# Kernel tuning notes

Hardware: AMD Instinct MI355X
Metric: run time of the kernel (lower is better)

Reference implementation:

```python
import jax, jax.numpy as jnp
import numpy as np

B, T, A, OBS = 4096, 32, 4, 115
H, K, ACT = 64, 8, 19
FEAT = 4 + 3 + 4 * A          # 23 structured features
IN_DIM = FEAT + ACT * A       # 99 with action one-hots


def setup_inputs() -> dict:
    key = jax.random.key(0)
    ks = jax.random.split(key, 16)
    s = lambda *sh: 1.0 / np.sqrt(sh[-1])
    inp = {
        "obs_seq": jax.random.normal(ks[0], (B, T, A, OBS), jnp.float32),
        "action_seq": jax.random.randint(ks[1], (B, T, A), 0, ACT, jnp.int32),
        # feature_proj: Linear(IN_DIM->H) + LayerNorm(H)
        "proj_W": jax.random.normal(ks[2], (H, IN_DIM), jnp.float32) * s(H, IN_DIM),
        "proj_b": jnp.zeros((H,), jnp.float32),
        "ln_g": jnp.ones((H,), jnp.float32),
        "ln_b": jnp.zeros((H,), jnp.float32),
        # 2-layer GRU
        "Wih0": jax.random.normal(ks[3], (3 * H, H), jnp.float32) * s(1, H),
        "Whh0": jax.random.normal(ks[4], (3 * H, H), jnp.float32) * s(1, H),
        "bih0": jnp.zeros((3 * H,), jnp.float32),
        "bhh0": jnp.zeros((3 * H,), jnp.float32),
        "Wih1": jax.random.normal(ks[5], (3 * H, H), jnp.float32) * s(1, H),
        "Whh1": jax.random.normal(ks[6], (3 * H, H), jnp.float32) * s(1, H),
        "bih1": jnp.zeros((3 * H,), jnp.float32),
        "bhh1": jnp.zeros((3 * H,), jnp.float32),
        # classifier MLP
        "cls_W1": jax.random.normal(ks[7], (H, H), jnp.float32) * s(H, H),
        "cls_b1": jnp.zeros((H,), jnp.float32),
        "cls_W2": jax.random.normal(ks[8], (K, H), jnp.float32) * s(K, H),
        "cls_b2": jnp.zeros((K,), jnp.float32),
    }
    return inp


def _extract_features(obs_seq, action_seq):
    b, t, a = obs_seq.shape[:3]
    # ball position from player 0's obs, and its finite-difference velocity
    ball_pos = obs_seq[:, :, 0, 88:90]                       # [B,T,2]
    ball_vel = jnp.concatenate(
        [jnp.zeros_like(ball_pos[:, :1]), ball_pos[:, 1:] - ball_pos[:, :-1]], axis=1)
    pos = obs_seq[..., 0:2]                                   # [B,T,A,2]
    pos_flat = pos.reshape(b, t, a * 2)
    centroid = pos.mean(axis=2)                               # [B,T,2]
    spread = jnp.sqrt(((pos - centroid[:, :, None]) ** 2).sum(-1).mean(2, keepdims=True) + 1e-6)
    # closest-teammate relative position: vectorized argmin over pairwise dists
    diff = pos[:, :, :, None, :] - pos[:, :, None, :, :]      # [B,T,A,A,2]
    d2 = (diff ** 2).sum(-1)                                  # [B,T,A,A]
    d2 = jnp.where(jnp.eye(a, dtype=bool), jnp.inf, d2)       # exclude self
    idx = jnp.argmin(d2, axis=-1)                             # [B,T,A]
    nearest = jnp.take_along_axis(pos, idx[..., None], axis=2)  # [B,T,A,2]
    closest_rel = (nearest - pos).reshape(b, t, a * 2)
    onehot = jax.nn.one_hot(action_seq, ACT, dtype=jnp.float32).reshape(b, t, a * ACT)
    return jnp.concatenate(
        [ball_pos, ball_vel, pos_flat, centroid, spread, closest_rel, onehot], axis=-1)


def _gru_layer(x_tbh, Wih, Whh, bih, bhh):
    h0 = jnp.zeros((x_tbh.shape[1], Whh.shape[1]), x_tbh.dtype)

    def step(h, x):
        gi = x @ Wih.T + bih
        gh = h @ Whh.T + bhh
        ir, iz, inn = jnp.split(gi, 3, axis=-1)
        hr, hz, hn = jnp.split(gh, 3, axis=-1)
        r = jax.nn.sigmoid(ir + hr)
        z = jax.nn.sigmoid(iz + hz)
        n = jnp.tanh(inn + r * hn)
        h_new = (1.0 - z) * n + z * h
        return h_new, h_new

    h_last, ys = jax.lax.scan(step, h0, x_tbh)
    return ys, h_last


def reference(obs_seq, action_seq, proj_W, proj_b, ln_g, ln_b,
              Wih0, Whh0, bih0, bhh0, Wih1, Whh1, bih1, bhh1,
              cls_W1, cls_b1, cls_W2, cls_b2):
    feats = _extract_features(obs_seq, action_seq)            # [B,T,99]
    x = feats @ proj_W.T + proj_b                             # [B,T,H]
    mu = x.mean(-1, keepdims=True)
    var = x.var(-1, keepdims=True)
    x = (x - mu) * jax.lax.rsqrt(var + 1e-5) * ln_g + ln_b
    x = jax.nn.relu(x)
    x = jnp.swapaxes(x, 0, 1)                                 # [T,B,H]
    ys0, _ = _gru_layer(x, Wih0, Whh0, bih0, bhh0)
    _, h_last = _gru_layer(ys0, Wih1, Whh1, bih1, bhh1)       # [B,H]
    hid = jax.nn.relu(h_last @ cls_W1.T + cls_b1)
    logits = hid @ cls_W2.T + cls_b2                          # [B,K]
    return logits
```

## Files before the change

### kernel.cpp

```cpp
#include <hip/hip_runtime.h>

#define B_ 4096
#define T_ 32
#define A_ 4
#define OBS_ 115
#define H_ 64
#define IN_DIM_ 99
#define ACT_ 19
#define NBT (B_*T_)

typedef _Float16 f16;
typedef _Float16 f16x8 __attribute__((ext_vector_type(8)));
typedef float f32x4 __attribute__((ext_vector_type(4)));

static __device__ __forceinline__ float sigmoid_f(float x) {
    return __builtin_amdgcn_rcpf(1.f + __expf(-x));
}
static __device__ __forceinline__ float tanh_f(float x) {
    return 1.f - 2.f * __builtin_amdgcn_rcpf(1.f + __expf(2.f * x));
}
static __device__ __forceinline__ f32x4 mfma16(f16x8 a, f16x8 b, f32x4 c) {
    return __builtin_amdgcn_mfma_f32_16x16x32_f16(a, b, c, 0, 0, 0);
}

__global__ __launch_bounds__(512, 1) void fused_all(
        const float* __restrict__ obs, const int* __restrict__ act,
        const float* __restrict__ projW, const float* __restrict__ pb,
        const float* __restrict__ lng, const float* __restrict__ lnb,
        const float* __restrict__ Wih0, const float* __restrict__ Whh0,
        const float* __restrict__ bih0, const float* __restrict__ bhh0,
        const float* __restrict__ Wih1, const float* __restrict__ Whh1,
        const float* __restrict__ bih1, const float* __restrict__ bhh1,
        const float* __restrict__ W1, const float* __restrict__ b1,
        const float* __restrict__ W2, const float* __restrict__ b2,
        float* __restrict__ out) {
    __shared__ float fl[512 * 25];
    __shared__ float wtl[IN_DIM_ * 64];
    __shared__ int al[512];
    __shared__ __align__(16) f16 xls[32 * 16 * 72];
    __shared__ __align__(16) f16 hbuf[2][2][16 * 72];

    int tid = threadIdx.x;
    int lane = tid & 63;
    int wv = __builtin_amdgcn_readfirstlane(tid >> 6);
    int c = lane & 15, q = lane >> 4;
    int rowbase = blockIdx.x * 16;

    auto ldw = [&](const float* W, int row0, int kcol) -> f16x8 {
        const float* p = W + (size_t)(row0 + c) * 64 + kcol + q * 8;
        f32x4 w0 = *(const f32x4*)p;
        f32x4 w1 = *(const f32x4*)(p + 4);
        f16x8 r;
        r[0] = (f16)w0[0]; r[1] = (f16)w0[1]; r[2] = (f16)w0[2]; r[3] = (f16)w0[3];
        r[4] = (f16)w1[0]; r[5] = (f16)w1[1]; r[6] = (f16)w1[2]; r[7] = (f16)w1[3];
        return r;
    };
    int L = wv >> 2;
    int S = (wv & 3) * 16;
    const float* Wih = L ? Wih1 : Wih0;
    const float* Whh = L ? Whh1 : Whh0;
    const float* bih = L ? bih1 : bih0;
    const float* bhh = L ? bhh1 : bhh0;
    f16x8 wih[3][2], whh[3][2];
#pragma unroll
    for (int g = 0; g < 3; g++)
#pragma unroll
        for (int kf = 0; kf < 2; kf++) {
            wih[g][kf] = ldw(Wih, g * 64 + S, kf * 32);
            whh[g][kf] = ldw(Whh, g * 64 + S, kf * 32);
        }
    float br = bih[S + c] + bhh[S + c];
    float bz = bih[64 + S + c] + bhh[64 + S + c];
    float bi = bih[128 + S + c];
    float bh = bhh[128 + S + c];
    f32x4 vbr = {br, br, br, br}, vbz = {bz, bz, bz, bz};
    f32x4 vbi = {bi, bi, bi, bi}, vbh = {bh, bh, bh, bh};

    {
        int n = blockIdx.x * 512 + tid;
        const float* o = obs + (size_t)n * (A_ * OBS_);
        float px[A_], py[A_];
#pragma unroll
        for (int a = 0; a < A_; a++) {
            float2 p2 = *(const float2*)&o[a * OBS_];
            px[a] = p2.x; py[a] = p2.y;
        }
        float2 bl = *(const float2*)&o[88];
        int t0 = tid & 31;
        float2 pbl = bl;
        if (t0 > 0) pbl = *(const float2*)&o[88 - A_ * OBS_];

        float cx = (px[0] + px[1] + px[2] + px[3]) * 0.25f;
        float cy = (py[0] + py[1] + py[2] + py[3]) * 0.25f;
        float sp = 0.f;
#pragma unroll
        for (int a = 0; a < A_; a++) { float dx = px[a] - cx, dy = py[a] - cy; sp += dx * dx + dy * dy; }
        sp = sqrtf(sp * 0.25f + 1e-6f);

        float crx[A_], cry[A_];
#pragma unroll
        for (int i = 0; i < A_; i++) {
            float best = 3.4e38f; int bj = 0;
#pragma unroll
            for (int j = 0; j < A_; j++) {
                if (j == i) continue;
                float dx = px[i] - px[j], dy = py[i] - py[j];
                float d2 = dx * dx + dy * dy;
                if (d2 < best) { best = d2; bj = j; }
            }
            crx[i] = px[bj] - px[i]; cry[i] = py[bj] - py[i];
        }

        float* f = &fl[tid * 25];
        f[0] = bl.x; f[1] = bl.y; f[2] = bl.x - pbl.x; f[3] = bl.y - pbl.y;
#pragma unroll
        for (int a = 0; a < A_; a++) { f[4 + 2 * a] = px[a]; f[5 + 2 * a] = py[a]; }
        f[12] = cx; f[13] = cy; f[14] = sp;
#pragma unroll
        for (int a = 0; a < A_; a++) { f[15 + 2 * a] = crx[a]; f[16 + 2 * a] = cry[a]; }

        int4 av = *(const int4*)&act[n * A_];
        al[tid] = av.x | (av.y << 8) | (av.z << 16) | (av.w << 24);

        for (int k = tid; k < IN_DIM_ * 64; k += 512) {
            int h = k / 64, i = k & 63;
            int hh = k / IN_DIM_, ii = k - hh * IN_DIM_;
            (void)h; (void)i;
            wtl[ii * 64 + hh] = projW[k];
        }
        for (int k = tid; k < 2 * 2 * 16 * 72; k += 512) ((f16*)hbuf)[k] = (f16)0.f;
    }
    __syncthreads();

    {
        float wc[23];
#pragma unroll
        for (int i = 0; i < 23; i++) wc[i] = wtl[i * 64 + lane];
        float pbv = pb[lane], g = lng[lane], bb = lnb[lane];

        for (int it = 0; it < 64; it++) {
            int lb = wv * 64 + it;
            int r = lb >> 5, t = lb & 31;
            const float* fp = &fl[lb * 25];
            float v = pbv;
#pragma unroll
            for (int i = 0; i < 23; i++) v += fp[i] * wc[i];
            int a4 = al[lb];
#pragma unroll
            for (int a = 0; a < A_; a++) {
                int ai = (a4 >> (8 * a)) & 0xFF;
                v += wtl[(23 + a * ACT_ + ai) * 64 + lane];
            }
            float s = v, ss = v * v;
#pragma unroll
            for (int m = 1; m < 64; m <<= 1) {
                s += __shfl_xor(s, m, 64);
                ss += __shfl_xor(ss, m, 64);
            }
            float mean = s * (1.f / 64.f);
            float var = ss * (1.f / 64.f) - mean * mean;
            float xn = (v - mean) * rsqrtf(var + 1e-5f) * g + bb;
            xn = fmaxf(xn, 0.f);
            xls[(t * 16 + r) * 72 + lane] = (f16)xn;
        }
    }
    __syncthreads();

    f32x4 hc = {0.f, 0.f, 0.f, 0.f};
    int p = 0;
    for (int i = 0; i <= T_; i++) {
        f16x8 hh0, hh1, in0, in1;
        if (L == 0) {
            hh0 = *(const f16x8*)&hbuf[0][p][c * 72 + q * 8];
            hh1 = *(const f16x8*)&hbuf[0][p][c * 72 + 32 + q * 8];
            int t = (i < T_) ? i : (T_ - 1);
            in0 = *(const f16x8*)&xls[(t * 16 + c) * 72 + q * 8];
            in1 = *(const f16x8*)&xls[(t * 16 + c) * 72 + 32 + q * 8];
        } else {
            hh0 = *(const f16x8*)&hbuf[1][p][c * 72 + q * 8];
            hh1 = *(const f16x8*)&hbuf[1][p][c * 72 + 32 + q * 8];
            in0 = *(const f16x8*)&hbuf[0][p][c * 72 + q * 8];
            in1 = *(const f16x8*)&hbuf[0][p][c * 72 + 32 + q * 8];
        }
        bool active = L ? (i > 0) : (i < T_);
        if (active) {
            f32x4 r = vbr, z = vbz, in_ = vbi, hn = vbh;
            r = mfma16(hh0, whh[0][0], r); r = mfma16(hh1, whh[0][1], r);
            r = mfma16(in0, wih[0][0], r); r = mfma16(in1, wih[0][1], r);
            z = mfma16(hh0, whh[1][0], z); z = mfma16(hh1, whh[1][1], z);
            z = mfma16(in0, wih[1][0], z); z = mfma16(in1, wih[1][1], z);
            in_ = mfma16(in0, wih[2][0], in_); in_ = mfma16(in1, wih[2][1], in_);
            hn = mfma16(hh0, whh[2][0], hn); hn = mfma16(hh1, whh[2][1], hn);
#pragma unroll
            for (int rr = 0; rr < 4; rr++) {
                float rg = sigmoid_f(r[rr]);
                float zg = sigmoid_f(z[rr]);
                float ng = tanh_f(in_[rr] + rg * hn[rr]);
                hc[rr] = ng + zg * (hc[rr] - ng);
            }
        }
#pragma unroll
        for (int rr = 0; rr < 4; rr++)
            hbuf[L][p ^ 1][(q * 4 + rr) * 72 + S + c] = (f16)hc[rr];
        __syncthreads();
        p ^= 1;
    }

    f16x8 ha0 = *(const f16x8*)&hbuf[1][p][c * 72 + q * 8];
    f16x8 ha1 = *(const f16x8*)&hbuf[1][p][c * 72 + 32 + q * 8];
    if (L == 0) {
        f16x8 w1f0 = ldw(W1, S, 0), w1f1 = ldw(W1, S, 32);
        float bw1 = b1[S + c];
        f32x4 hid = {bw1, bw1, bw1, bw1};
        hid = mfma16(ha0, w1f0, hid);
        hid = mfma16(ha1, w1f1, hid);
#pragma unroll
        for (int rr = 0; rr < 4; rr++) {
            float hv = fmaxf(hid[rr], 0.f);
            hbuf[0][p ^ 1][(q * 4 + rr) * 72 + S + c] = (f16)hv;
        }
    }
    __syncthreads();
    if (wv == 0) {
        f16x8 ga0 = *(const f16x8*)&hbuf[0][p ^ 1][c * 72 + q * 8];
        f16x8 ga1 = *(const f16x8*)&hbuf[0][p ^ 1][c * 72 + 32 + q * 8];
        f16x8 w2f0 = {}, w2f1 = {};
        float bo = 0.f;
        if (c < 8) {
            w2f0 = ldw(W2, 0, 0);
            w2f1 = ldw(W2, 0, 32);
            bo = b2[c];
        }
        f32x4 lg = {bo, bo, bo, bo};
        lg = mfma16(ga0, w2f0, lg);
        lg = mfma16(ga1, w2f1, lg);
        if (c < 8) {
#pragma unroll
            for (int rr = 0; rr < 4; rr++)
                out[(size_t)(rowbase + q * 4 + rr) * 8 + c] = lg[rr];
        }
    }
}

extern "C" void kernel_launch(void* const* d_in, const int* in_sizes, int n_in,
                              void* d_out, int out_size, void* d_ws, size_t ws_size,
                              hipStream_t stream) {
    const float* obs  = (const float*)d_in[0];
    const int*   act  = (const int*)d_in[1];
    const float* projW = (const float*)d_in[2];
    const float* projb = (const float*)d_in[3];
    const float* lng  = (const float*)d_in[4];
    const float* lnb  = (const float*)d_in[5];
    const float* Wih0 = (const float*)d_in[6];
    const float* Whh0 = (const float*)d_in[7];
    const float* bih0 = (const float*)d_in[8];
    const float* bhh0 = (const float*)d_in[9];
    const float* Wih1 = (const float*)d_in[10];
    const float* Whh1 = (const float*)d_in[11];
    const float* bih1 = (const float*)d_in[12];
    const float* bhh1 = (const float*)d_in[13];
    const float* W1   = (const float*)d_in[14];
    const float* b1   = (const float*)d_in[15];
    const float* W2   = (const float*)d_in[16];
    const float* b2   = (const float*)d_in[17];
    float* out = (float*)d_out;

    fused_all<<<B_ / 16, 512, 0, stream>>>(obs, act, projW, projb, lng, lnb,
                                           Wih0, Whh0, bih0, bhh0,
                                           Wih1, Whh1, bih1, bhh1,
                                           W1, b1, W2, b2, out);
}
```

Baseline: 387.0 us.

## Keep projection features in registers and broadcast via readlane with DPP LayerNorm reduction

Per-thread structured features and packed action indices now stay in VGPRs instead of going through shared memory. The projection loop broadcasts each row's features with readlane, which drops the fl/al LDS arrays and their reads. The previous-step ball position now comes from a warp shuffle rather than a second global load. The transposed weight table is padded to 65 columns to avoid bank conflicts, and the LayerNorm sum reductions use DPP row shifts and row_bcast instead of shfl_xor. Register pressure rises from the 23-float feature array, and the shuffle correctness relies on each 32-lane group mapping to one sequence.

```diff
diff --git a/kernel.cpp b/kernel.cpp
--- a/kernel.cpp
+++ b/kernel.cpp
@@ -21,6 +21,14 @@
 }
 static __device__ __forceinline__ f32x4 mfma16(f16x8 a, f16x8 b, f32x4 c) {
     return __builtin_amdgcn_mfma_f32_16x16x32_f16(a, b, c, 0, 0, 0);
+}
+static __device__ __forceinline__ float rlf(float x, int l) {
+    return __int_as_float(__builtin_amdgcn_readlane(__float_as_int(x), l));
+}
+template <int CTRL, int RM>
+static __device__ __forceinline__ float dpp_add(float x) {
+    int y = __builtin_amdgcn_update_dpp(0, __float_as_int(x), CTRL, RM, 0xf, true);
+    return x + __int_as_float(y);
 }
 
 __global__ __launch_bounds__(512, 1) void fused_all(
@@ -34,9 +42,7 @@
         const float* __restrict__ W1, const float* __restrict__ b1,
         const float* __restrict__ W2, const float* __restrict__ b2,
         float* __restrict__ out) {
-    __shared__ float fl[512 * 25];
-    __shared__ float wtl[IN_DIM_ * 64];
-    __shared__ int al[512];
+    __shared__ float wtl[IN_DIM_ * 65];
     __shared__ __align__(16) f16 xls[32 * 16 * 72];
     __shared__ __align__(16) f16 hbuf[2][2][16 * 72];
 
@@ -76,6 +82,8 @@
     f32x4 vbr = {br, br, br, br}, vbz = {bz, bz, bz, bz};
     f32x4 vbi = {bi, bi, bi, bi}, vbh = {bh, bh, bh, bh};
 
+    float fr[23];
+    int a4;
     {
         int n = blockIdx.x * 512 + tid;
         const float* o = obs + (size_t)n * (A_ * OBS_);
@@ -86,9 +94,8 @@
             px[a] = p2.x; py[a] = p2.y;
         }
         float2 bl = *(const float2*)&o[88];
-        int t0 = tid & 31;
-        float2 pbl = bl;
-        if (t0 > 0) pbl = *(const float2*)&o[88 - A_ * OBS_];
+        float pblx = __shfl_up(bl.x, 1, 32);
+        float pbly = __shfl_up(bl.y, 1, 32);
 
         float cx = (px[0] + px[1] + px[2] + px[3]) * 0.25f;
         float cy = (py[0] + py[1] + py[2] + py[3]) * 0.25f;
@@ -97,7 +104,10 @@
         for (int a = 0; a < A_; a++) { float dx = px[a] - cx, dy = py[a] - cy; sp += dx * dx + dy * dy; }
         sp = sqrtf(sp * 0.25f + 1e-6f);
 
-        float crx[A_], cry[A_];
+        fr[0] = bl.x; fr[1] = bl.y; fr[2] = bl.x - pblx; fr[3] = bl.y - pbly;
+#pragma unroll
+        for (int a = 0; a < A_; a++) { fr[4 + 2 * a] = px[a]; fr[5 + 2 * a] = py[a]; }
+        fr[12] = cx; fr[13] = cy; fr[14] = sp;
 #pragma unroll
         for (int i = 0; i < A_; i++) {
             float best = 3.4e38f; int bj = 0;
@@ -108,25 +118,15 @@
                 float d2 = dx * dx + dy * dy;
                 if (d2 < best) { best = d2; bj = j; }
             }
-            crx[i] = px[bj] - px[i]; cry[i] = py[bj] - py[i];
-        }
-
-        float* f = &fl[tid * 25];
-        f[0] = bl.x; f[1] = bl.y; f[2] = bl.x - pbl.x; f[3] = bl.y - pbl.y;
-#pragma unroll
-        for (int a = 0; a < A_; a++) { f[4 + 2 * a] = px[a]; f[5 + 2 * a] = py[a]; }
-        f[12] = cx; f[13] = cy; f[14] = sp;
-#pragma unroll
-        for (int a = 0; a < A_; a++) { f[15 + 2 * a] = crx[a]; f[16 + 2 * a] = cry[a]; }
+            fr[15 + 2 * i] = px[bj] - px[i]; fr[16 + 2 * i] = py[bj] - py[i];
+        }
 
         int4 av = *(const int4*)&act[n * A_];
-        al[tid] = av.x | (av.y << 8) | (av.z << 16) | (av.w << 24);
+        a4 = av.x | (av.y << 8) | (av.z << 16) | (av.w << 24);
 
         for (int k = tid; k < IN_DIM_ * 64; k += 512) {
-            int h = k / 64, i = k & 63;
             int hh = k / IN_DIM_, ii = k - hh * IN_DIM_;
-            (void)h; (void)i;
-            wtl[ii * 64 + hh] = projW[k];
+            wtl[ii * 65 + hh] = projW[k];
         }
         for (int k = tid; k < 2 * 2 * 16 * 72; k += 512) ((f16*)hbuf)[k] = (f16)0.f;
     }
@@ -135,30 +135,42 @@
     {
         float wc[23];
 #pragma unroll
-        for (int i = 0; i < 23; i++) wc[i] = wtl[i * 64 + lane];
+        for (int i = 0; i < 23; i++) wc[i] = wtl[i * 65 + lane];
         float pbv = pb[lane], g = lng[lane], bb = lnb[lane];
 
+#pragma unroll 2
         for (int it = 0; it < 64; it++) {
             int lb = wv * 64 + it;
             int r = lb >> 5, t = lb & 31;
-            const float* fp = &fl[lb * 25];
-            float v = pbv;
-#pragma unroll
-            for (int i = 0; i < 23; i++) v += fp[i] * wc[i];
-            int a4 = al[lb];
-#pragma unroll
-            for (int a = 0; a < A_; a++) {
-                int ai = (a4 >> (8 * a)) & 0xFF;
-                v += wtl[(23 + a * ACT_ + ai) * 64 + lane];
+            int a4i = __builtin_amdgcn_readlane(a4, it);
+            float oh0 = wtl[(23 + 0 * ACT_ + (a4i & 0xFF)) * 65 + lane];
+            float oh1 = wtl[(23 + 1 * ACT_ + ((a4i >> 8) & 0xFF)) * 65 + lane];
+            float oh2 = wtl[(23 + 2 * ACT_ + ((a4i >> 16) & 0xFF)) * 65 + lane];
+            float oh3 = wtl[(23 + 3 * ACT_ + ((a4i >> 24) & 0xFF)) * 65 + lane];
+            float ac0 = 0.f, ac1 = 0.f, ac2 = 0.f, ac3 = 0.f;
+#pragma unroll
+            for (int i = 0; i < 20; i += 4) {
+                ac0 += rlf(fr[i + 0], it) * wc[i + 0];
+                ac1 += rlf(fr[i + 1], it) * wc[i + 1];
+                ac2 += rlf(fr[i + 2], it) * wc[i + 2];
+                ac3 += rlf(fr[i + 3], it) * wc[i + 3];
             }
+            ac0 += rlf(fr[20], it) * wc[20];
+            ac1 += rlf(fr[21], it) * wc[21];
+            ac2 += rlf(fr[22], it) * wc[22];
+            float v = pbv + ((ac0 + ac1) + (ac2 + ac3)) + ((oh0 + oh1) + (oh2 + oh3));
+
             float s = v, ss = v * v;
-#pragma unroll
-            for (int m = 1; m < 64; m <<= 1) {
-                s += __shfl_xor(s, m, 64);
-                ss += __shfl_xor(ss, m, 64);
-            }
-            float mean = s * (1.f / 64.f);
-            float var = ss * (1.f / 64.f) - mean * mean;
+            s = dpp_add<0x111, 0xf>(s);  ss = dpp_add<0x111, 0xf>(ss);
+            s = dpp_add<0x112, 0xf>(s);  ss = dpp_add<0x112, 0xf>(ss);
+            s = dpp_add<0x114, 0xf>(s);  ss = dpp_add<0x114, 0xf>(ss);
+            s = dpp_add<0x118, 0xf>(s);  ss = dpp_add<0x118, 0xf>(ss);
+            s = dpp_add<0x142, 0xa>(s);  ss = dpp_add<0x142, 0xa>(ss);
+            s = dpp_add<0x143, 0xc>(s);  ss = dpp_add<0x143, 0xc>(ss);
+            float stot = rlf(s, 63), sstot = rlf(ss, 63);
+
+            float mean = stot * (1.f / 64.f);
+            float var = sstot * (1.f / 64.f) - mean * mean;
             float xn = (v - mean) * rsqrtf(var + 1e-5f) * g + bb;
             xn = fmaxf(xn, 0.f);
             xls[(t * 16 + r) * 72 + lane] = (f16)xn;
```

Measured after the change: 379.8 us. Within noise of the previous version (-1.9%).

## Compute feature projection with fp16 MFMA and shuffle-based ball velocity

Applied to the files above, without the earlier changes.

Replaces the per-lane scalar 23-feature dot product in the projection stage with 16x16x32 f16 MFMA tiles. Features are stored as padded f16 rows and the first 23 projection weight columns are kept as an f16 copy in shared memory. The one-hot action weights are padded to stride 65 to avoid bank conflicts, and the LayerNorm reduction now spans 16 lanes across 4 column tiles. The previous-timestep ball position comes from a warp shuffle instead of a second global load. This adds fp16 rounding to the projection inputs and weights.

```diff
diff --git a/kernel.cpp b/kernel.cpp
--- a/kernel.cpp
+++ b/kernel.cpp
@@ -34,8 +34,9 @@
         const float* __restrict__ W1, const float* __restrict__ b1,
         const float* __restrict__ W2, const float* __restrict__ b2,
         float* __restrict__ out) {
-    __shared__ float fl[512 * 25];
-    __shared__ float wtl[IN_DIM_ * 64];
+    __shared__ float wtl[IN_DIM_ * 65];
+    __shared__ __align__(16) f16 flh[512 * 32];
+    __shared__ __align__(16) f16 pjw16[64 * 32];
     __shared__ int al[512];
     __shared__ __align__(16) f16 xls[32 * 16 * 72];
     __shared__ __align__(16) f16 hbuf[2][2][16 * 72];
@@ -86,9 +87,8 @@
             px[a] = p2.x; py[a] = p2.y;
         }
         float2 bl = *(const float2*)&o[88];
-        int t0 = tid & 31;
-        float2 pbl = bl;
-        if (t0 > 0) pbl = *(const float2*)&o[88 - A_ * OBS_];
+        float pblx = __shfl_up(bl.x, 1, 32);
+        float pbly = __shfl_up(bl.y, 1, 32);
 
         float cx = (px[0] + px[1] + px[2] + px[3]) * 0.25f;
         float cy = (py[0] + py[1] + py[2] + py[3]) * 0.25f;
@@ -97,7 +97,11 @@
         for (int a = 0; a < A_; a++) { float dx = px[a] - cx, dy = py[a] - cy; sp += dx * dx + dy * dy; }
         sp = sqrtf(sp * 0.25f + 1e-6f);
 
-        float crx[A_], cry[A_];
+        float fr[23];
+        fr[0] = bl.x; fr[1] = bl.y; fr[2] = bl.x - pblx; fr[3] = bl.y - pbly;
+#pragma unroll
+        for (int a = 0; a < A_; a++) { fr[4 + 2 * a] = px[a]; fr[5 + 2 * a] = py[a]; }
+        fr[12] = cx; fr[13] = cy; fr[14] = sp;
 #pragma unroll
         for (int i = 0; i < A_; i++) {
             float best = 3.4e38f; int bj = 0;
@@ -108,60 +112,85 @@
                 float d2 = dx * dx + dy * dy;
                 if (d2 < best) { best = d2; bj = j; }
             }
-            crx[i] = px[bj] - px[i]; cry[i] = py[bj] - py[i];
-        }
-
-        float* f = &fl[tid * 25];
-        f[0] = bl.x; f[1] = bl.y; f[2] = bl.x - pbl.x; f[3] = bl.y - pbl.y;
-#pragma unroll
-        for (int a = 0; a < A_; a++) { f[4 + 2 * a] = px[a]; f[5 + 2 * a] = py[a]; }
-        f[12] = cx; f[13] = cy; f[14] = sp;
-#pragma unroll
-        for (int a = 0; a < A_; a++) { f[15 + 2 * a] = crx[a]; f[16 + 2 * a] = cry[a]; }
+            fr[15 + 2 * i] = px[bj] - px[i]; fr[16 + 2 * i] = py[bj] - py[i];
+        }
 
         int4 av = *(const int4*)&act[n * A_];
         al[tid] = av.x | (av.y << 8) | (av.z << 16) | (av.w << 24);
 
+        f16x8 p0, p1, p2, p3 = {};
+#pragma unroll
+        for (int i = 0; i < 8; i++) { p0[i] = (f16)fr[i]; p1[i] = (f16)fr[8 + i]; }
+#pragma unroll
+        for (int i = 0; i < 7; i++) p2[i] = (f16)fr[16 + i];
+        p2[7] = (f16)0.f;
+        *(f16x8*)&flh[tid * 32]      = p0;
+        *(f16x8*)&flh[tid * 32 + 8]  = p1;
+        *(f16x8*)&flh[tid * 32 + 16] = p2;
+        *(f16x8*)&flh[tid * 32 + 24] = p3;
+
         for (int k = tid; k < IN_DIM_ * 64; k += 512) {
-            int h = k / 64, i = k & 63;
             int hh = k / IN_DIM_, ii = k - hh * IN_DIM_;
-            (void)h; (void)i;
-            wtl[ii * 64 + hh] = projW[k];
+            wtl[ii * 65 + hh] = projW[k];
+        }
+        for (int k = tid; k < 64 * 32; k += 512) {
+            int h = k >> 5, kk = k & 31;
+            pjw16[k] = (kk < 23) ? (f16)projW[h * IN_DIM_ + kk] : (f16)0.f;
         }
         for (int k = tid; k < 2 * 2 * 16 * 72; k += 512) ((f16*)hbuf)[k] = (f16)0.f;
     }
     __syncthreads();
 
     {
-        float wc[23];
-#pragma unroll
-        for (int i = 0; i < 23; i++) wc[i] = wtl[i * 64 + lane];
-        float pbv = pb[lane], g = lng[lane], bb = lnb[lane];
-
-        for (int it = 0; it < 64; it++) {
-            int lb = wv * 64 + it;
-            int r = lb >> 5, t = lb & 31;
-            const float* fp = &fl[lb * 25];
-            float v = pbv;
-#pragma unroll
-            for (int i = 0; i < 23; i++) v += fp[i] * wc[i];
-            int a4 = al[lb];
-#pragma unroll
-            for (int a = 0; a < A_; a++) {
-                int ai = (a4 >> (8 * a)) & 0xFF;
-                v += wtl[(23 + a * ACT_ + ai) * 64 + lane];
+        float pbv[4], gg[4], bbv[4];
+        f16x8 bfr[4];
+#pragma unroll
+        for (int tl = 0; tl < 4; tl++) {
+            int col = tl * 16 + c;
+            pbv[tl] = pb[col]; gg[tl] = lng[col]; bbv[tl] = lnb[col];
+            bfr[tl] = *(const f16x8*)&pjw16[col * 32 + q * 8];
+        }
+#pragma unroll
+        for (int rt = 0; rt < 4; rt++) {
+            int row0 = wv * 64 + rt * 16;
+            f16x8 af = *(const f16x8*)&flh[(row0 + c) * 32 + q * 8];
+            f32x4 z4 = {0.f, 0.f, 0.f, 0.f};
+            f32x4 a0 = mfma16(af, bfr[0], z4);
+            f32x4 a1 = mfma16(af, bfr[1], z4);
+            f32x4 a2 = mfma16(af, bfr[2], z4);
+            f32x4 a3 = mfma16(af, bfr[3], z4);
+#pragma unroll
+            for (int rr = 0; rr < 4; rr++) {
+                int lb = row0 + q * 4 + rr;
+                int a4i = al[lb];
+                float v0 = a0[rr] + pbv[0];
+                float v1 = a1[rr] + pbv[1];
+                float v2 = a2[rr] + pbv[2];
+                float v3 = a3[rr] + pbv[3];
+#pragma unroll
+                for (int a = 0; a < 4; a++) {
+                    const float* wrow =
+                        &wtl[(23 + a * ACT_ + ((a4i >> (8 * a)) & 0xFF)) * 65 + c];
+                    v0 += wrow[0]; v1 += wrow[16]; v2 += wrow[32]; v3 += wrow[48];
+                }
+                float s = (v0 + v1) + (v2 + v3);
+                float ss = v0 * v0 + v1 * v1 + v2 * v2 + v3 * v3;
+#pragma unroll
+                for (int m = 1; m < 16; m <<= 1) {
+                    s += __shfl_xor(s, m, 64);
+                    ss += __shfl_xor(ss, m, 64);
+                }
+                float mean = s * (1.f / 64.f);
+                float var = ss * (1.f / 64.f) - mean * mean;
+                float rs = rsqrtf(var + 1e-5f);
+                int t = lb & 31, r = lb >> 5;
+                f16* xrow = &xls[(t * 16 + r) * 72];
+                float xn;
+                xn = fmaxf((v0 - mean) * rs * gg[0] + bbv[0], 0.f); xrow[c]      = (f16)xn;
+                xn = fmaxf((v1 - mean) * rs * gg[1] + bbv[1], 0.f); xrow[16 + c] = (f16)xn;
+                xn = fmaxf((v2 - mean) * rs * gg[2] + bbv[2], 0.f); xrow[32 + c] = (f16)xn;
+                xn = fmaxf((v3 - mean) * rs * gg[3] + bbv[3], 0.f); xrow[48 + c] = (f16)xn;
             }
-            float s = v, ss = v * v;
-#pragma unroll
-            for (int m = 1; m < 64; m <<= 1) {
-                s += __shfl_xor(s, m, 64);
-                ss += __shfl_xor(ss, m, 64);
-            }
-            float mean = s * (1.f / 64.f);
-            float var = ss * (1.f / 64.f) - mean * mean;
-            float xn = (v - mean) * rsqrtf(var + 1e-5f) * g + bb;
-            xn = fmaxf(xn, 0.f);
-            xls[(t * 16 + r) * 72 + lane] = (f16)xn;
         }
     }
     __syncthreads();
```

New measurement: 353.1 us. 8.8% less time.
